# Optimization experiments

Hardware: AMD Instinct MI355X
Metric: run time of the kernel (lower is better)

## Reference

```python
import jax, jax.numpy as jnp
import numpy as np

B, N, K, D, H, L = 2, 2048, 256, 768, 256, 64
REL_PROP = 3
NUM_BUCKETS = 64


def _pair_scores(u, dist_feat, left_w, left_b, right_w, right_b, out_w, out_b):
    # OptFFpairs-style pairwise scorer: left(u)_i + right(u)_j + dist_emb -> relu -> out
    left = jnp.einsum('bkd,hd->bkh', u, left_w) + left_b    # [B,K,H]
    right = jnp.einsum('bkd,hd->bkh', u, right_w) + right_b  # [B,K,H]
    h = jax.nn.relu(left[:, :, None, :] + right[:, None, :, :] + dist_feat)  # [B,K,K,H]
    return jnp.einsum('bijh,lh->bijl', h, out_w) + out_b     # [B,K,K,L]


def setup_inputs():
    key = jax.random.key(0)
    ks = jax.random.split(key, 12)
    s = 0.02
    all_span_vecs = jax.random.normal(ks[0], (B, N, D), dtype=jnp.float32)
    span_vecs = jax.random.normal(ks[1], (B, K, D), dtype=jnp.float32)
    span_begin = jnp.sort(jax.random.randint(ks[2], (B, K), 0, 1000), axis=-1).astype(jnp.int32)
    span_end = (span_begin + jax.random.randint(ks[3], (B, K), 1, 16)).astype(jnp.int32)
    square_mask = jnp.ones((B, K, K), dtype=jnp.float32)
    span_lengths = jnp.full((B,), float(K), dtype=jnp.float32)
    prune_indices = jnp.stack([
        jnp.sort(jax.random.choice(jax.random.fold_in(ks[4], b), N, (K,), replace=False))
        for b in range(B)
    ]).astype(jnp.int32)
    return {
        'all_span_vecs': all_span_vecs, 'span_vecs': span_vecs,
        'span_begin': span_begin, 'span_end': span_end,
        'square_mask': square_mask, 'span_lengths': span_lengths,
        'prune_indices': prune_indices,
        'left_w': jax.random.normal(ks[5], (H, D)) * s, 'left_b': jnp.zeros((H,), jnp.float32),
        'right_w': jax.random.normal(ks[6], (H, D)) * s, 'right_b': jnp.zeros((H,), jnp.float32),
        'dist_emb': jax.random.normal(ks[7], (NUM_BUCKETS, H)) * s,
        'out_w': jax.random.normal(ks[8], (L, H)) * s, 'out_b': jnp.zeros((L,), jnp.float32),
        'A_w': jax.random.normal(ks[9], (D, L)) * s,
        'B_w': jax.random.normal(ks[10], (D, L)) * s,
        'gate_w': jax.random.normal(ks[11], (D, 2 * D)) * s, 'gate_b': jnp.zeros((D,), jnp.float32),
    }


def reference(all_span_vecs, span_vecs, span_begin, span_end, square_mask, span_lengths,
              prune_indices, left_w, left_b, right_w, right_b, dist_emb, out_w, out_b,
              A_w, B_w, gate_w, gate_b):
    # distance-bucket embedding of the span pair (span_pair_generator)
    dist = span_begin[:, None, :] - span_end[:, :, None]                 # [B,K,K]
    buckets = jnp.clip(jnp.abs(dist), 0, NUM_BUCKETS - 1)
    dist_feat = dist_emb[buckets]                                        # [B,K,K,H]
    inv_len = 1.0 / span_lengths[:, None, None]                          # [B,1,1]

    update = span_vecs
    scores = _pair_scores(update, dist_feat, left_w, left_b, right_w, right_b, out_w, out_b)
    for _ in range(REL_PROP):
        probs = jax.nn.sigmoid(scores) * square_mask[..., None]          # [B,K,K,L]
        # torch: (A(probs) * update.unsqueeze(-2)).sum(-3) -> sum over i (rows)
        ctxt1 = jnp.einsum('bijl,dl,bid->bjd', probs, A_w, update) * inv_len
        # torch: (B(probs) * update.unsqueeze(-3)).sum(-2) -> sum over j (cols)
        ctxt2 = jnp.einsum('bijl,dl,bjd->bid', probs, B_w, update) * inv_len
        c = ctxt1 + ctxt2
        # MyGate: sigmoid-gated convex combination of old state and context
        g = jax.nn.sigmoid(jnp.concatenate([update, c], axis=-1) @ gate_w.T + gate_b)
        update = g * update + (1.0 - g) * c
        scores = _pair_scores(update, dist_feat, left_w, left_b, right_w, right_b, out_w, out_b)

    # overwrite_spans: scatter updated filtered spans back into the full span tensor
    valid = jnp.arange(K)[None, :] < span_lengths[:, None]               # [B,K]
    old = jnp.take_along_axis(all_span_vecs, prune_indices[..., None], axis=1)
    vals = jnp.where(valid[..., None], update, old)
    bidx = jnp.arange(B)[:, None]
    new_all = all_span_vecs.at[bidx, prune_indices].set(vals)
    return new_all, update, scores
```

## Files before the change

kernel.cpp:

```cpp
#include <hip/hip_runtime.h>

#define B_ 2
#define N_ 2048
#define K_ 256
#define D_ 768
#define H_ 256
#define L_ 64
#define BK_ (B_*K_)

typedef __attribute__((ext_vector_type(8))) __bf16 bf16x8;
typedef __attribute__((ext_vector_type(8))) unsigned short ushort8;
typedef __attribute__((ext_vector_type(4))) unsigned short ushort4v;
typedef __attribute__((ext_vector_type(4))) float f32x4;

__device__ __forceinline__ float sigm(float x) { return 1.0f / (1.0f + __expf(-x)); }

__device__ __forceinline__ unsigned short f2b(float f) {
    union { float f; unsigned int u; } v; v.f = f;
    unsigned int u = v.u;
    return (unsigned short)((u + 0x7FFFu + ((u >> 16) & 1u)) >> 16);
}
__device__ __forceinline__ unsigned short f2bc(float f) {
    __bf16 h = (__bf16)f;
    return __builtin_bit_cast(unsigned short, h);
}
__device__ __forceinline__ float b2f(unsigned short us) {
    union { unsigned int u; float f; } v; v.u = ((unsigned int)us) << 16;
    return v.f;
}
__device__ __forceinline__ bf16x8 ldb(const unsigned short* p) {
    ushort8 v = *(const ushort8*)p;
    return __builtin_bit_cast(bf16x8, v);
}

__global__ __launch_bounds__(256) void conv_all(
    const float* __restrict__ lw, const float* __restrict__ rw,
    const float* __restrict__ ow, const float* __restrict__ gw,
    const float* __restrict__ aw, const float* __restrict__ bw,
    const float* __restrict__ sv, const float* __restrict__ de,
    unsigned short* __restrict__ lwb, unsigned short* __restrict__ rwb,
    unsigned short* __restrict__ owb, unsigned short* __restrict__ gwb,
    unsigned short* __restrict__ wab, unsigned short* __restrict__ wbb,
    unsigned short* __restrict__ ub, unsigned short* __restrict__ deb)
{
    int i4 = (blockIdx.x * 256 + threadIdx.x) * 4;
    const float* src; unsigned short* dst; int off;
    if      (i4 <  196608) { src = lw; dst = lwb; off = 0; }
    else if (i4 <  393216) { src = rw; dst = rwb; off = 196608; }
    else if (i4 <  409600) { src = ow; dst = owb; off = 393216; }
    else if (i4 < 1589248) { src = gw; dst = gwb; off = 409600; }
    else if (i4 < 1638400) { src = aw; dst = wab; off = 1589248; }
    else if (i4 < 1687552) { src = bw; dst = wbb; off = 1638400; }
    else if (i4 < 2080768) { src = sv; dst = ub;  off = 1687552; }
    else if (i4 < 2097152) { src = de; dst = deb; off = 2080768; }
    else return;
    int j = i4 - off;
    float4 v = *(const float4*)&src[j];
    ushort4v p; p.x = f2b(v.x); p.y = f2b(v.y); p.z = f2b(v.z); p.w = f2b(v.w);
    *(ushort4v*)&dst[j] = p;
}

__global__ __launch_bounds__(256) void conv_c(
    const float* __restrict__ c, unsigned short* __restrict__ cb)
{
    int i = (blockIdx.x * 256 + threadIdx.x) * 4;
    float4 v = *(const float4*)&c[i];
    ushort4v p; p.x = f2b(v.x); p.y = f2b(v.y); p.z = f2b(v.z); p.w = f2b(v.w);
    *(ushort4v*)&cb[i] = p;
}

__global__ __launch_bounds__(64) void lr_mfma2(
    const unsigned short* __restrict__ Ub,
    const unsigned short* __restrict__ lwb, const float* __restrict__ lb,
    const unsigned short* __restrict__ rwb, const float* __restrict__ rb,
    float* __restrict__ outL, float* __restrict__ outR)
{
    const int side = blockIdx.z;
    const unsigned short* __restrict__ W = side ? rwb : lwb;
    const float* __restrict__ bias = side ? rb : lb;
    float* __restrict__ outp = side ? outR : outL;
    const int r0 = blockIdx.x * 16, n0 = blockIdx.y * 16;
    const int lane = threadIdx.x;
    const int col = lane & 15, quad = lane >> 4;
    const unsigned short* arow = &Ub[(size_t)(r0 + col)*D_ + quad*8];
    const unsigned short* brow = &W[(size_t)(n0 + col)*D_ + quad*8];
    f32x4 acc = {};
    #pragma unroll
    for (int kc = 0; kc < D_; kc += 32) {
        bf16x8 a = ldb(arow + kc);
        bf16x8 bb = ldb(brow + kc);
        acc = __builtin_amdgcn_mfma_f32_16x16x32_bf16(a, bb, acc, 0, 0, 0);
    }
    const int n = n0 + col;
    const float bv = bias[n];
    #pragma unroll
    for (int r = 0; r < 4; ++r)
        outp[(size_t)(r0 + quad*4 + r)*H_ + n] = acc[r] + bv;
}

__global__ __launch_bounds__(256, 2) void scores_v9(
    const float* __restrict__ leftb, const float* __restrict__ rightb,
    const int* __restrict__ span_begin, const int* __restrict__ span_end,
    const unsigned short* __restrict__ deb, const unsigned short* __restrict__ owb,
    const float* __restrict__ out_b, const float* __restrict__ mask,
    float* __restrict__ S, unsigned short* __restrict__ Pt, int writeP)
{
    const int j0 = blockIdx.x * 64;
    const int i0 = blockIdx.y * 8;
    const int b  = blockIdx.z;
    const int tid = threadIdx.x;
    const int w = tid >> 6, lane = tid & 63, col = lane & 15, quad = lane >> 4;
    const int jrow = w*16 + col;

    __shared__ unsigned short sDe[64][272];
    __shared__ float sL[8][256];
    __shared__ float sT[64][68];
    __shared__ float sMask[8][64];
    __shared__ int   sBkt[8][64];

    #pragma unroll
    for (int q = 0; q < 8; ++q) {
        int c = tid + q*256;
        int row = c >> 5, seg = (c & 31) * 8;
        *(ushort8*)&sDe[row][seg] = *(const ushort8*)&deb[row*H_ + seg];
    }
    #pragma unroll
    for (int q = 0; q < 2; ++q) {
        int p = tid + q*256;
        int ii = p >> 6, jj = p & 63;
        int d = span_begin[b*K_ + j0 + jj] - span_end[b*K_ + i0 + ii];
        if (d < 0) d = -d;
        sBkt[ii][jj] = d > 63 ? 63 : d;
        sMask[ii][jj] = mask[(size_t)(b*K_ + i0 + ii)*K_ + j0 + jj];
    }
    #pragma unroll
    for (int q = 0; q < 2; ++q) {
        int f = tid + q*256;
        int row = f >> 6, c4 = (f & 63) * 4;
        *(float4*)&sL[row][c4] = *(const float4*)&leftb[(size_t)(b*K_ + i0 + row)*H_ + c4];
    }
    __syncthreads();

    const unsigned short* sDeF = &sDe[0][0];
    int deoff[8];
    #pragma unroll
    for (int i = 0; i < 8; ++i) deoff[i] = sBkt[i][jrow] * 272;

    const float* rrow = &rightb[(size_t)(b*K_ + j0 + jrow)*H_ + quad*8];

    f32x4 acc[8][4] = {};
    #pragma unroll
    for (int k = 0; k < 8; ++k) {
        const float4 r0 = *(const float4*)&rrow[k*32];
        const float4 r1 = *(const float4*)&rrow[k*32 + 4];
        bf16x8 bbk[4];
        #pragma unroll
        for (int lt = 0; lt < 4; ++lt)
            bbk[lt] = ldb(&owb[(size_t)(lt*16 + col)*H_ + k*32 + quad*8]);
        #pragma unroll
        for (int i = 0; i < 8; ++i) {
            const ushort8 dv = *(const ushort8*)&sDeF[deoff[i] + k*32 + quad*8];
            const float* lr = &sL[i][k*32 + quad*8];
            const float4 l0 = *(const float4*)lr;
            const float4 l1 = *(const float4*)(lr + 4);
            bf16x8 a;
            a[0] = (__bf16)fmaxf(0.f, l0.x + r0.x + b2f(dv[0]));
            a[1] = (__bf16)fmaxf(0.f, l0.y + r0.y + b2f(dv[1]));
            a[2] = (__bf16)fmaxf(0.f, l0.z + r0.z + b2f(dv[2]));
            a[3] = (__bf16)fmaxf(0.f, l0.w + r0.w + b2f(dv[3]));
            a[4] = (__bf16)fmaxf(0.f, l1.x + r1.x + b2f(dv[4]));
            a[5] = (__bf16)fmaxf(0.f, l1.y + r1.y + b2f(dv[5]));
            a[6] = (__bf16)fmaxf(0.f, l1.z + r1.z + b2f(dv[6]));
            a[7] = (__bf16)fmaxf(0.f, l1.w + r1.w + b2f(dv[7]));
            #pragma unroll
            for (int lt = 0; lt < 4; ++lt)
                acc[i][lt] = __builtin_amdgcn_mfma_f32_16x16x32_bf16(a, bbk[lt], acc[i][lt], 0, 0, 0);
        }
    }

    float ob[4];
    #pragma unroll
    for (int lt = 0; lt < 4; ++lt) ob[lt] = out_b[lt*16 + col];

    #pragma unroll
    for (int i = 0; i < 8; ++i) {
        __syncthreads();
        #pragma unroll
        for (int lt = 0; lt < 4; ++lt)
            #pragma unroll
            for (int r = 0; r < 4; ++r)
                sT[w*16 + quad*4 + r][lt*16 + col] = acc[i][lt][r] + ob[lt];
        __syncthreads();
        const int jj = tid >> 2, seg = (tid & 3) * 16;
        const int j = j0 + jj, ii = i0 + i;
        if (writeP) {
            const float msk = sMask[i][jj];
            ushort8 o0, o1;
            #pragma unroll
            for (int e = 0; e < 8; ++e) {
                o0[e] = f2bc(sigm(sT[jj][seg + e]) * msk);
                o1[e] = f2bc(sigm(sT[jj][seg + 8 + e]) * msk);
            }
            unsigned short* dst = &Pt[(((size_t)b*K_ + j)*K_ + ii)*L_ + seg];
            *(ushort8*)&dst[0] = o0;
            *(ushort8*)&dst[8] = o1;
        } else {
            float* dst = &S[(((size_t)b*K_ + ii)*K_ + j)*L_ + seg];
            #pragma unroll
            for (int q2 = 0; q2 < 4; ++q2) {
                float4 v;
                v.x = sT[jj][seg + q2*4 + 0];
                v.y = sT[jj][seg + q2*4 + 1];
                v.z = sT[jj][seg + q2*4 + 2];
                v.w = sT[jj][seg + q2*4 + 3];
                *(float4*)&dst[q2*4] = v;
            }
        }
    }
}

__global__ __launch_bounds__(512, 4) void ctxt_v7(
    const unsigned short* __restrict__ Pt, const float* __restrict__ U,
    const unsigned short* __restrict__ WAb, const unsigned short* __restrict__ WBb,
    const float* __restrict__ lens, float* __restrict__ cacc)
{
    const int bid = blockIdx.x;
    const int m0 = (bid & 15) << 4;
    const int t0 = ((bid >> 4) & 7) << 5;
    const int mode = (bid >> 7) & 1;
    const int b = bid >> 8;
    const unsigned short* __restrict__ Wb = mode ? WBb : WAb;
    const int tid = threadIdx.x;
    const int w = tid >> 6, lane = tid & 63, col = lane & 15, quad = lane >> 4;
    const int dbase = w * 96;

    __shared__ unsigned short sP[2][16][72];
    __shared__ float sU[2][768];

    bf16x8 bw[6][2];
    #pragma unroll
    for (int dt = 0; dt < 6; ++dt)
        #pragma unroll
        for (int kc = 0; kc < 2; ++kc)
            bw[dt][kc] = ldb(&Wb[(size_t)(dbase + dt*16 + col)*L_ + kc*32 + quad*8]);

    const bool doP = tid < 128;
    const bool doU = (tid >= 128) && (tid < 320);
    const int prow = (tid & 127) >> 3, pseg = (tid & 7) * 8;
    const int ucol = (tid - 128) * 4;
    size_t pbase, tstep;
    if (mode) { pbase = (((size_t)b*K_ + t0)*K_ + m0 + prow)*L_ + pseg; tstep = (size_t)K_*L_; }
    else      { pbase = (((size_t)b*K_ + m0 + prow)*K_ + t0)*L_ + pseg; tstep = (size_t)L_; }

    ushort8 pvA, pvB; float4 uvA, uvB;
    if (doP) { pvA = *(const ushort8*)&Pt[pbase];
               pvB = *(const ushort8*)&Pt[pbase + tstep]; }
    if (doU) { uvA = *(const float4*)&U[((size_t)b*K_ + t0)*D_ + ucol];
               uvB = *(const float4*)&U[((size_t)b*K_ + t0 + 1)*D_ + ucol]; }

    f32x4 acc[6] = {};

    #define CTXT_COMPUTE(BUFI)                                                    \
    {                                                                             \
        bf16x8 a0 = ldb(&sP[BUFI][col][quad*8]);                                  \
        bf16x8 a1 = ldb(&sP[BUFI][col][32 + quad*8]);                             \
        _Pragma("unroll")                                                         \
        for (int dt = 0; dt < 6; ++dt) {                                          \
            f32x4 g = {0.f, 0.f, 0.f, 0.f};                                       \
            g = __builtin_amdgcn_mfma_f32_16x16x32_bf16(a0, bw[dt][0], g, 0, 0, 0); \
            g = __builtin_amdgcn_mfma_f32_16x16x32_bf16(a1, bw[dt][1], g, 0, 0, 0); \
            const float uu = sU[BUFI][dbase + dt*16 + col];                       \
            acc[dt] += g * uu;                                                    \
        }                                                                         \
    }

    for (int t = 0; t < 32; t += 2) {
        if (doP) *(ushort8*)&sP[0][prow][pseg] = pvA;
        if (doU) *(float4*)&sU[0][ucol] = uvA;
        __syncthreads();
        if (t + 2 < 32) {
            if (doP) pvA = *(const ushort8*)&Pt[pbase + (size_t)(t + 2)*tstep];
            if (doU) uvA = *(const float4*)&U[((size_t)b*K_ + t0 + t + 2)*D_ + ucol];
        }
        CTXT_COMPUTE(0)
        if (doP) *(ushort8*)&sP[1][prow][pseg] = pvB;
        if (doU) *(float4*)&sU[1][ucol] = uvB;
        __syncthreads();
        if (t + 3 < 32) {
            if (doP) pvB = *(const ushort8*)&Pt[pbase + (size_t)(t + 3)*tstep];
            if (doU) uvB = *(const float4*)&U[((size_t)b*K_ + t0 + t + 3)*D_ + ucol];
        }
        CTXT_COMPUTE(1)
    }
    #undef CTXT_COMPUTE

    const float inv_len = 1.0f / lens[b];
    #pragma unroll
    for (int dt = 0; dt < 6; ++dt)
        #pragma unroll
        for (int r = 0; r < 4; ++r) {
            const int m = m0 + quad*4 + r;
            atomicAdd(&cacc[((size_t)(b*K_) + m)*D_ + dbase + dt*16 + col],
                      acc[dt][r] * inv_len);
        }
}

__global__ __launch_bounds__(64) void gate_mfma2(
    const unsigned short* __restrict__ Ub, const unsigned short* __restrict__ cb,
    const unsigned short* __restrict__ gwb, const float* __restrict__ gb,
    const float* __restrict__ Ucur, const float* __restrict__ Cc,
    float* __restrict__ Unext, unsigned short* __restrict__ Ubnext)
{
    const int r0 = blockIdx.x * 16, n0 = blockIdx.y * 16;
    const int lane = threadIdx.x;
    const int col = lane & 15, quad = lane >> 4;
    const unsigned short* arow_u = &Ub[(size_t)(r0 + col)*D_ + quad*8];
    const unsigned short* arow_c = &cb[(size_t)(r0 + col)*D_ + quad*8];
    const unsigned short* brow   = &gwb[(size_t)(n0 + col)*(2*D_) + quad*8];
    f32x4 acc = {};
    #pragma unroll
    for (int kc = 0; kc < D_; kc += 32) {
        bf16x8 a = ldb(arow_u + kc);
        bf16x8 bb = ldb(brow + kc);
        acc = __builtin_amdgcn_mfma_f32_16x16x32_bf16(a, bb, acc, 0, 0, 0);
    }
    #pragma unroll
    for (int kc = 0; kc < D_; kc += 32) {
        bf16x8 a = ldb(arow_c + kc);
        bf16x8 bb = ldb(brow + D_ + kc);
        acc = __builtin_amdgcn_mfma_f32_16x16x32_bf16(a, bb, acc, 0, 0, 0);
    }
    const int n = n0 + col;
    const float gbv = gb[n];
    #pragma unroll
    for (int r = 0; r < 4; ++r) {
        const size_t idx = (size_t)(r0 + quad*4 + r)*D_ + n;
        const float gg = sigm(acc[r] + gbv);
        const float o = gg * Ucur[idx] + (1.f - gg) * Cc[idx];
        Unext[idx] = o;
        Ubnext[idx] = f2b(o);
    }
}

__global__ __launch_bounds__(256) void scatter_kernel(
    const float* __restrict__ upd, const int* __restrict__ prune,
    const float* __restrict__ lens, float* __restrict__ out_all)
{
    const int blk = blockIdx.x;
    const int b = blk / K_, k = blk % K_;
    if ((float)k < lens[b]) {
        const int pi = prune[b*K_ + k];
        const int tid = threadIdx.x;
        if (tid < D_/4) {
            float4 v = *(const float4*)&upd[((size_t)b*K_ + k)*D_ + tid*4];
            *(float4*)&out_all[((size_t)b*N_ + pi)*D_ + tid*4] = v;
        }
    }
}

extern "C" void kernel_launch(void* const* d_in, const int* in_sizes, int n_in,
                              void* d_out, int out_size, void* d_ws, size_t ws_size,
                              hipStream_t stream) {
    (void)in_sizes; (void)n_in; (void)out_size; (void)ws_size;
    const float* all_span_vecs = (const float*)d_in[0];
    const float* span_vecs     = (const float*)d_in[1];
    const int*   span_begin    = (const int*)d_in[2];
    const int*   span_end      = (const int*)d_in[3];
    const float* mask          = (const float*)d_in[4];
    const float* lens          = (const float*)d_in[5];
    const int*   prune         = (const int*)d_in[6];
    const float* lw  = (const float*)d_in[7];
    const float* lb  = (const float*)d_in[8];
    const float* rw  = (const float*)d_in[9];
    const float* rb  = (const float*)d_in[10];
    const float* dist_emb = (const float*)d_in[11];
    const float* out_w    = (const float*)d_in[12];
    const float* out_b    = (const float*)d_in[13];
    const float* A_w = (const float*)d_in[14];
    const float* B_w = (const float*)d_in[15];
    const float* gw  = (const float*)d_in[16];
    const float* gb  = (const float*)d_in[17];

    float* out_all = (float*)d_out;
    float* out_upd = out_all + (size_t)B_*N_*D_;
    float* out_sc  = out_upd + (size_t)BK_*D_;

    float* ws     = (float*)d_ws;
    float* leftb  = ws;
    float* rightf = leftb + (size_t)BK_*H_;
    float* U0     = rightf + (size_t)BK_*H_;
    float* U1     = U0 + (size_t)BK_*D_;
    float* cbuf   = U1 + (size_t)BK_*D_;
    unsigned short* WAb = (unsigned short*)(cbuf + (size_t)BK_*D_);
    unsigned short* WBb = WAb + (size_t)D_*L_;
    unsigned short* lwb = WBb + (size_t)D_*L_;
    unsigned short* rwb = lwb + (size_t)H_*D_;
    unsigned short* owb = rwb + (size_t)H_*D_;
    unsigned short* gwb = owb + (size_t)L_*H_;
    unsigned short* deb = gwb + (size_t)D_*2*D_;
    unsigned short* Ub0 = deb + (size_t)64*H_;
    unsigned short* Ub1 = Ub0 + (size_t)BK_*D_;
    unsigned short* cb  = Ub1 + (size_t)BK_*D_;
    unsigned short* Pt  = cb + (size_t)BK_*D_;

    hipMemcpyAsync(out_all, all_span_vecs, sizeof(float)*(size_t)B_*N_*D_,
                   hipMemcpyDeviceToDevice, stream);

    dim3 blk256(256), blk64(64), blk512(512);
    conv_all<<<dim3(2048), blk256, 0, stream>>>(lw, rw, out_w, gw, A_w, B_w, span_vecs, dist_emb,
                                                lwb, rwb, owb, gwb, WAb, WBb, Ub0, deb);
    lr_mfma2<<<dim3(BK_/16, H_/16, 2), blk64, 0, stream>>>(Ub0, lwb, lb, rwb, rb, leftb, rightf);
    scores_v9<<<dim3(K_/64, K_/8, B_), blk256, 0, stream>>>(leftb, rightf, span_begin, span_end,
                                                            deb, owb, out_b, mask,
                                                            out_sc, Pt, 1);
    const float* Ucur = span_vecs;
    const unsigned short* Ubcur = Ub0;
    float* nexts[3] = {U0, U1, out_upd};
    unsigned short* nextsUb[3] = {Ub1, Ub0, Ub1};
    for (int it = 0; it < 3; ++it) {
        hipMemsetAsync(cbuf, 0, sizeof(float)*(size_t)BK_*D_, stream);
        ctxt_v7<<<dim3(512), blk512, 0, stream>>>(Pt, Ucur, WAb, WBb, lens, cbuf);
        conv_c<<<dim3(BK_*D_/1024), blk256, 0, stream>>>(cbuf, cb);
        gate_mfma2<<<dim3(BK_/16, D_/16), blk64, 0, stream>>>(Ubcur, cb, gwb, gb,
                                                              Ucur, cbuf, nexts[it], nextsUb[it]);
        Ucur = nexts[it];
        Ubcur = nextsUb[it];
        lr_mfma2<<<dim3(BK_/16, H_/16, 2), blk64, 0, stream>>>(Ubcur, lwb, lb, rwb, rb, leftb, rightf);
        scores_v9<<<dim3(K_/64, K_/8, B_), blk256, 0, stream>>>(leftb, rightf, span_begin, span_end,
                                                                deb, owb, out_b, mask,
                                                                out_sc, Pt, it == 2 ? 0 : 1);
    }
    scatter_kernel<<<dim3(BK_), blk256, 0, stream>>>(out_upd, prune, lens, out_all);
}
```

Measured before the change: 428.8 us.

## Read fp32 distance embedding from global in scores kernel, halve i-tile per block

The scores kernel no longer stages the bf16 distance-embedding table in shared memory. It reads the fp32 dist_emb rows straight from global memory (L1/L2 cached), so the bf16 conversion of that table is dropped from conv_all. The i-tile per block shrinks from 8 to 4, which doubles the grid and halves accumulator registers, and the min-blocks launch bound is removed. This cuts per-block LDS use and the 34KB table preload, which should raise occupancy and parallelism. The cost is gathered global loads of twice the byte width per element and more redundant right/out_w loads across blocks.

After: 451.5 us. 5.3% more time.

```diff
diff --git a/kernel.cpp b/kernel.cpp
--- a/kernel.cpp
+++ b/kernel.cpp
@@ -37,11 +37,11 @@
     const float* __restrict__ lw, const float* __restrict__ rw,
     const float* __restrict__ ow, const float* __restrict__ gw,
     const float* __restrict__ aw, const float* __restrict__ bw,
-    const float* __restrict__ sv, const float* __restrict__ de,
+    const float* __restrict__ sv,
     unsigned short* __restrict__ lwb, unsigned short* __restrict__ rwb,
     unsigned short* __restrict__ owb, unsigned short* __restrict__ gwb,
     unsigned short* __restrict__ wab, unsigned short* __restrict__ wbb,
-    unsigned short* __restrict__ ub, unsigned short* __restrict__ deb)
+    unsigned short* __restrict__ ub)
 {
     int i4 = (blockIdx.x * 256 + threadIdx.x) * 4;
     const float* src; unsigned short* dst; int off;
@@ -52,7 +52,6 @@
     else if (i4 < 1638400) { src = aw; dst = wab; off = 1589248; }
     else if (i4 < 1687552) { src = bw; dst = wbb; off = 1638400; }
     else if (i4 < 2080768) { src = sv; dst = ub;  off = 1687552; }
-    else if (i4 < 2097152) { src = de; dst = deb; off = 2080768; }
     else return;
     int j = i4 - off;
     float4 v = *(const float4*)&src[j];
@@ -98,57 +97,45 @@
         outp[(size_t)(r0 + quad*4 + r)*H_ + n] = acc[r] + bv;
 }
 
-__global__ __launch_bounds__(256, 2) void scores_v9(
+__global__ __launch_bounds__(256) void scores_v10(
     const float* __restrict__ leftb, const float* __restrict__ rightb,
     const int* __restrict__ span_begin, const int* __restrict__ span_end,
-    const unsigned short* __restrict__ deb, const unsigned short* __restrict__ owb,
+    const float* __restrict__ de, const unsigned short* __restrict__ owb,
     const float* __restrict__ out_b, const float* __restrict__ mask,
     float* __restrict__ S, unsigned short* __restrict__ Pt, int writeP)
 {
     const int j0 = blockIdx.x * 64;
-    const int i0 = blockIdx.y * 8;
+    const int i0 = blockIdx.y * 4;
     const int b  = blockIdx.z;
     const int tid = threadIdx.x;
     const int w = tid >> 6, lane = tid & 63, col = lane & 15, quad = lane >> 4;
     const int jrow = w*16 + col;
 
-    __shared__ unsigned short sDe[64][272];
-    __shared__ float sL[8][256];
+    __shared__ float sL[4][256];
     __shared__ float sT[64][68];
-    __shared__ float sMask[8][64];
-    __shared__ int   sBkt[8][64];
-
-    #pragma unroll
-    for (int q = 0; q < 8; ++q) {
-        int c = tid + q*256;
-        int row = c >> 5, seg = (c & 31) * 8;
-        *(ushort8*)&sDe[row][seg] = *(const ushort8*)&deb[row*H_ + seg];
-    }
-    #pragma unroll
-    for (int q = 0; q < 2; ++q) {
-        int p = tid + q*256;
-        int ii = p >> 6, jj = p & 63;
+    __shared__ float sMask[4][64];
+    __shared__ int   sBkt[4][64];
+
+    {
+        int ii = tid >> 6, jj = tid & 63;
         int d = span_begin[b*K_ + j0 + jj] - span_end[b*K_ + i0 + ii];
         if (d < 0) d = -d;
         sBkt[ii][jj] = d > 63 ? 63 : d;
         sMask[ii][jj] = mask[(size_t)(b*K_ + i0 + ii)*K_ + j0 + jj];
     }
-    #pragma unroll
-    for (int q = 0; q < 2; ++q) {
-        int f = tid + q*256;
-        int row = f >> 6, c4 = (f & 63) * 4;
+    {
+        int row = tid >> 6, c4 = (tid & 63) * 4;
         *(float4*)&sL[row][c4] = *(const float4*)&leftb[(size_t)(b*K_ + i0 + row)*H_ + c4];
     }
     __syncthreads();
 
-    const unsigned short* sDeF = &sDe[0][0];
-    int deoff[8];
-    #pragma unroll
-    for (int i = 0; i < 8; ++i) deoff[i] = sBkt[i][jrow] * 272;
+    int deoff[4];
+    #pragma unroll
+    for (int i = 0; i < 4; ++i) deoff[i] = sBkt[i][jrow] * H_;
 
     const float* rrow = &rightb[(size_t)(b*K_ + j0 + jrow)*H_ + quad*8];
 
-    f32x4 acc[8][4] = {};
+    f32x4 acc[4][4] = {};
     #pragma unroll
     for (int k = 0; k < 8; ++k) {
         const float4 r0 = *(const float4*)&rrow[k*32];
@@ -158,20 +145,22 @@
         for (int lt = 0; lt < 4; ++lt)
             bbk[lt] = ldb(&owb[(size_t)(lt*16 + col)*H_ + k*32 + quad*8]);
         #pragma unroll
-        for (int i = 0; i < 8; ++i) {
-            const ushort8 dv = *(const ushort8*)&sDeF[deoff[i] + k*32 + quad*8];
+        for (int i = 0; i < 4; ++i) {
+            const float* dr = &de[deoff[i] + k*32 + quad*8];
+            const float4 d0 = *(const float4*)dr;
+            const float4 d1 = *(const float4*)(dr + 4);
             const float* lr = &sL[i][k*32 + quad*8];
             const float4 l0 = *(const float4*)lr;
             const float4 l1 = *(const float4*)(lr + 4);
             bf16x8 a;
-            a[0] = (__bf16)fmaxf(0.f, l0.x + r0.x + b2f(dv[0]));
-            a[1] = (__bf16)fmaxf(0.f, l0.y + r0.y + b2f(dv[1]));
-            a[2] = (__bf16)fmaxf(0.f, l0.z + r0.z + b2f(dv[2]));
-            a[3] = (__bf16)fmaxf(0.f, l0.w + r0.w + b2f(dv[3]));
-            a[4] = (__bf16)fmaxf(0.f, l1.x + r1.x + b2f(dv[4]));
-            a[5] = (__bf16)fmaxf(0.f, l1.y + r1.y + b2f(dv[5]));
-            a[6] = (__bf16)fmaxf(0.f, l1.z + r1.z + b2f(dv[6]));
-            a[7] = (__bf16)fmaxf(0.f, l1.w + r1.w + b2f(dv[7]));
+            a[0] = (__bf16)fmaxf(0.f, l0.x + r0.x + d0.x);
+            a[1] = (__bf16)fmaxf(0.f, l0.y + r0.y + d0.y);
+            a[2] = (__bf16)fmaxf(0.f, l0.z + r0.z + d0.z);
+            a[3] = (__bf16)fmaxf(0.f, l0.w + r0.w + d0.w);
+            a[4] = (__bf16)fmaxf(0.f, l1.x + r1.x + d1.x);
+            a[5] = (__bf16)fmaxf(0.f, l1.y + r1.y + d1.y);
+            a[6] = (__bf16)fmaxf(0.f, l1.z + r1.z + d1.z);
+            a[7] = (__bf16)fmaxf(0.f, l1.w + r1.w + d1.w);
             #pragma unroll
             for (int lt = 0; lt < 4; ++lt)
                 acc[i][lt] = __builtin_amdgcn_mfma_f32_16x16x32_bf16(a, bbk[lt], acc[i][lt], 0, 0, 0);
@@ -183,7 +172,7 @@
     for (int lt = 0; lt < 4; ++lt) ob[lt] = out_b[lt*16 + col];
 
     #pragma unroll
-    for (int i = 0; i < 8; ++i) {
+    for (int i = 0; i < 4; ++i) {
         __syncthreads();
         #pragma unroll
         for (int lt = 0; lt < 4; ++lt)
@@ -397,8 +386,7 @@
     unsigned short* rwb = lwb + (size_t)H_*D_;
     unsigned short* owb = rwb + (size_t)H_*D_;
     unsigned short* gwb = owb + (size_t)L_*H_;
-    unsigned short* deb = gwb + (size_t)D_*2*D_;
-    unsigned short* Ub0 = deb + (size_t)64*H_;
+    unsigned short* Ub0 = gwb + (size_t)D_*2*D_;
     unsigned short* Ub1 = Ub0 + (size_t)BK_*D_;
     unsigned short* cb  = Ub1 + (size_t)BK_*D_;
     unsigned short* Pt  = cb + (size_t)BK_*D_;
@@ -407,12 +395,12 @@
                    hipMemcpyDeviceToDevice, stream);
 
     dim3 blk256(256), blk64(64), blk512(512);
-    conv_all<<<dim3(2048), blk256, 0, stream>>>(lw, rw, out_w, gw, A_w, B_w, span_vecs, dist_emb,
-                                                lwb, rwb, owb, gwb, WAb, WBb, Ub0, deb);
+    conv_all<<<dim3(2032), blk256, 0, stream>>>(lw, rw, out_w, gw, A_w, B_w, span_vecs,
+                                                lwb, rwb, owb, gwb, WAb, WBb, Ub0);
     lr_mfma2<<<dim3(BK_/16, H_/16, 2), blk64, 0, stream>>>(Ub0, lwb, lb, rwb, rb, leftb, rightf);
-    scores_v9<<<dim3(K_/64, K_/8, B_), blk256, 0, stream>>>(leftb, rightf, span_begin, span_end,
-                                                            deb, owb, out_b, mask,
-                                                            out_sc, Pt, 1);
+    scores_v10<<<dim3(K_/64, K_/4, B_), blk256, 0, stream>>>(leftb, rightf, span_begin, span_end,
+                                                             dist_emb, owb, out_b, mask,
+                                                             out_sc, Pt, 1);
     const float* Ucur = span_vecs;
     const unsigned short* Ubcur = Ub0;
     float* nexts[3] = {U0, U1, out_upd};
@@ -426,9 +414,9 @@
         Ucur = nexts[it];
         Ubcur = nextsUb[it];
         lr_mfma2<<<dim3(BK_/16, H_/16, 2), blk64, 0, stream>>>(Ubcur, lwb, lb, rwb, rb, leftb, rightf);
-        scores_v9<<<dim3(K_/64, K_/8, B_), blk256, 0, stream>>>(leftb, rightf, span_begin, span_end,
-                                                                deb, owb, out_b, mask,
-                                                                out_sc, Pt, it == 2 ? 0 : 1);
+        scores_v10<<<dim3(K_/64, K_/4, B_), blk256, 0, stream>>>(leftb, rightf, span_begin, span_end,
+                                                                 dist_emb, owb, out_b, mask,
+                                                                 out_sc, Pt, it == 2 ? 0 : 1);
     }
     scatter_kernel<<<dim3(BK_), blk256, 0, stream>>>(out_upd, prune, lens, out_all);
 }
```
